# Optimization experiments

Measured on AMD Instinct MI355X. Metric: run time of the kernel, lower is better.

## Reference

```python
import jax, jax.numpy as jnp
import numpy as np

N, E, NNZ = 50000, 10000, 250000   # nodes, hyperedges, incidences
IN_CH, H, D = 128, 64, 6           # in_channels, MLP_hidden, stalk dim
EPS = 1e-5


def setup_inputs() -> dict:
    key = jax.random.key(0)
    ks = jax.random.split(key, 12)
    inp = {}
    inp["x"] = jax.random.normal(ks[0], (N, IN_CH), jnp.float32)
    inp["hyperedge_attr"] = jax.random.normal(ks[1], (E, IN_CH), jnp.float32)  # init_hedge='rand'
    inp["node_idx"] = jax.random.randint(ks[2], (NNZ,), 0, N)
    inp["edge_idx"] = jax.random.randint(ks[3], (NNZ,), 0, E)
    inp["node_types"] = jax.random.randint(ks[4], (N,), 0, 3)
    inp["hyperedge_types"] = jax.random.randint(ks[5], (E,), 0, 6)
    s = 1.0 / np.sqrt(IN_CH)
    inp["W_lin"] = jax.random.uniform(ks[6], (IN_CH, H * D), jnp.float32, -s, s)
    inp["b_lin"] = jnp.zeros((H * D,), jnp.float32)
    inp["ln_g"] = jnp.ones((2 * H,), jnp.float32)
    inp["ln_b"] = jnp.zeros((2 * H,), jnp.float32)
    s2 = 1.0 / np.sqrt(2 * H)
    inp["W_sheaf"] = jax.random.uniform(ks[7], (2 * H, D), jnp.float32, -s2, s2)
    inp["b_sheaf"] = jnp.zeros((D,), jnp.float32)
    s3 = 1.0 / np.sqrt(H)
    inp["W_conv0"] = jax.random.uniform(ks[8], (H, H), jnp.float32, -s3, s3)
    inp["b_conv0"] = jnp.zeros((H,), jnp.float32)
    inp["W_conv1"] = jax.random.uniform(ks[9], (H, H), jnp.float32, -s3, s3)
    inp["b_conv1"] = jnp.zeros((H,), jnp.float32)
    return inp


def _layernorm(x, g, b):
    mu = x.mean(-1, keepdims=True)
    var = ((x - mu) ** 2).mean(-1, keepdims=True)
    return (x - mu) * jax.lax.rsqrt(var + EPS) * g + b


def reference(x, hyperedge_attr, node_idx, edge_idx, node_types, hyperedge_types,
              W_lin, b_lin, ln_g, ln_b, W_sheaf, b_sheaf,
              W_conv0, b_conv0, W_conv1, b_conv1):
    # --- input projection + stalk reshape (self.lin) ---
    xs = (x @ W_lin + b_lin).reshape(N * D, H)              # [N*d, H]
    es = (hyperedge_attr @ W_lin + b_lin).reshape(E * D, H)  # [E*d, H]

    # --- SheafBuilderDiag (local_concat, sigmoid act) ---
    xa = xs.reshape(N, D, H).mean(1)   # [N, H] stalk-averaged node feats
    ea = es.reshape(E, D, H).mean(1)   # [E, H]
    feat = jnp.concatenate([xa[node_idx], ea[edge_idx]], axis=-1)  # [NNZ, 2H]
    alpha = jax.nn.sigmoid(_layernorm(feat, ln_g, ln_b) @ W_sheaf + b_sheaf)  # [NNZ, D]

    dr = jnp.arange(D)
    row_exp = (node_idx[:, None] * D + dr).reshape(-1)  # [NNZ*D] expanded node index
    col_exp = (edge_idx[:, None] * D + dr).reshape(-1)  # [NNZ*D] expanded hyperedge index
    a = alpha.reshape(-1)                               # [NNZ*D]

    # --- degree_norm: D^-1 (nodes) and B^-1 (hyperedges) from incidence counts ---
    ones = jnp.ones_like(a)
    Dn = jax.ops.segment_sum(ones, row_exp, num_segments=N * D)
    Dinv = jnp.where(Dn > 0, 1.0 / Dn, 0.0)
    Bn = jax.ops.segment_sum(ones, col_exp, num_segments=E * D)
    Binv = jnp.where(Bn > 0, 1.0 / Bn, 0.0)

    def conv(xin, W, bias):
        # HyperDiffusionDiagSheafConv: out = xW - D^-1 H^T B^-1 H (xW) + bias
        xl = xin @ W
        m = Binv[:, None] * jax.ops.segment_sum(a[:, None] * xl[row_exp], col_exp, num_segments=E * D)
        agg = Dinv[:, None] * jax.ops.segment_sum(a[:, None] * m[col_exp], row_exp, num_segments=N * D)
        return xl - agg + bias

    h1 = jax.nn.elu(conv(xs, W_conv0, b_conv0))   # dropout inactive (eval)
    h2 = conv(h1, W_conv1, b_conv1)
    return jax.nn.elu(h2.reshape(N, H * D))
```

## Files before the change

### kernel.cpp

```cpp
#include <hip/hip_runtime.h>
#include <hip/hip_bf16.h>

#define N_NODES 50000
#define N_EDGES 10000
#define NNZV    250000
#define IN_CH   128
#define HDIM    64
#define DSTALK  6
#define HD      384
#define NROWS   (N_NODES * DSTALK)
#define EROWS   (N_EDGES * DSTALK)

__global__ __launch_bounds__(256) void k_wefft(
    const float* __restrict__ W_lin, const float* __restrict__ W0,
    float* __restrict__ W0effT) {
  int idx = blockIdx.x * blockDim.x + threadIdx.x;
  if (idx >= IN_CH * HD) return;
  int k = idx / HD, j = idx - k * HD;
  int r = j >> 6, h = j & 63;
  float s = 0.f;
#pragma unroll 8
  for (int m = 0; m < HDIM; m++)
    s += W_lin[k * HD + r * HDIM + m] * W0[m * HDIM + h];
  W0effT[(size_t)j * IN_CH + k] = s;
}

#define WS_BASE (IN_CH * HDIM + HD + HDIM)
#define WS_END  (WS_BASE + 780 + HDIM * HDIM)
__global__ __launch_bounds__(256) void k_wsmall(
    const float* __restrict__ W_lin, const float* __restrict__ b_lin,
    const float* __restrict__ W0, const float* __restrict__ W1,
    const float* __restrict__ g, const float* __restrict__ bln,
    const float* __restrict__ Ws, const float* __restrict__ bs,
    float* __restrict__ Wm, float* __restrict__ cm, float* __restrict__ c0,
    float* __restrict__ gwN, float* __restrict__ gwE,
    float* __restrict__ G, float* __restrict__ K, float* __restrict__ W1T) {
  int idx = blockIdx.x * blockDim.x + threadIdx.x;
  if (idx < IN_CH * HDIM) {
    int k = idx >> 6, h = idx & 63;
    float s = 0.f;
#pragma unroll
    for (int r = 0; r < DSTALK; r++) s += W_lin[k * HD + r * HDIM + h];
    Wm[idx] = s * (1.f / 6.f);
  } else if (idx < IN_CH * HDIM + HD) {
    int j = idx - IN_CH * HDIM;
    int r = j >> 6, h = j & 63;
    float s = 0.f;
#pragma unroll 8
    for (int m = 0; m < HDIM; m++) s += b_lin[r * HDIM + m] * W0[m * HDIM + h];
    c0[j] = s;
  } else if (idx < WS_BASE) {
    int h = idx - IN_CH * HDIM - HD;
    float s = 0.f;
#pragma unroll
    for (int r = 0; r < DSTALK; r++) s += b_lin[r * HDIM + h];
    cm[h] = s * (1.f / 6.f);
  } else if (idx < WS_BASE + 384) {
    int i = idx - WS_BASE;
    int h = i / 6, r = i - h * 6;
    gwN[i] = g[h] * Ws[h * DSTALK + r];
  } else if (idx < WS_BASE + 768) {
    int i = idx - WS_BASE - 384;
    int h = i / 6, r = i - h * 6;
    gwE[i] = g[64 + h] * Ws[(64 + h) * DSTALK + r];
  } else if (idx < WS_BASE + 774) {
    int r = idx - WS_BASE - 768;
    float s = 0.f;
    for (int i = 0; i < 2 * HDIM; i++) s += g[i] * Ws[i * DSTALK + r];
    G[r] = s;
  } else if (idx < WS_BASE + 780) {
    int r = idx - WS_BASE - 774;
    float s = 0.f;
    for (int i = 0; i < 2 * HDIM; i++) s += bln[i] * Ws[i * DSTALK + r];
    K[r] = s + bs[r];
  } else if (idx < WS_END) {
    int i = idx - WS_BASE - 780;
    int c = i >> 6, k = i & 63;
    W1T[c * HDIM + k] = W1[k * HDIM + c];
  }
}

__global__ __launch_bounds__(256) void k_xa_stats(
    const float* __restrict__ x, const float* __restrict__ ea,
    const float* __restrict__ Wm, const float* __restrict__ cm,
    const float* __restrict__ gwN, const float* __restrict__ gwE,
    float* __restrict__ stats) {
  __shared__ float lx[64][IN_CH];
  __shared__ float ox[64][HDIM + 1];
  __shared__ float lgw[2][64 * DSTALK];
  const int row0 = blockIdx.x * 64;
  const int tid = threadIdx.x;
  for (int i = tid; i < 2 * 64 * DSTALK; i += 256) {
    int which = i / 384, k = i - which * 384;
    lgw[which][k] = which ? gwE[k] : gwN[k];
  }
  for (int i = tid; i < 64 * IN_CH; i += 256) {
    int r = i >> 7, k = i & 127;
    int row = row0 + r;
    float v = 0.f;
    if (row < N_NODES) v = x[row * IN_CH + k];
    else if (row < N_NODES + N_EDGES) v = ea[(row - N_NODES) * IN_CH + k];
    lx[r][k] = v;
  }
  __syncthreads();
  const int col = tid & 63, rg = tid >> 6;
  float acc[16];
#pragma unroll
  for (int i = 0; i < 16; i++) acc[i] = 0.f;
  for (int k = 0; k < IN_CH; k++) {
    float w = Wm[k * HDIM + col];
#pragma unroll
    for (int i = 0; i < 16; i++) acc[i] += lx[rg * 16 + i][k] * w;
  }
  const float c = cm[col];
#pragma unroll
  for (int i = 0; i < 16; i++) ox[rg * 16 + i][col] = acc[i] + c;
  __syncthreads();
  for (int t = tid; t < 512; t += 256) {
    int row = t >> 3, st = t & 7;
    int grow = row0 + row;
    if (grow >= N_NODES + N_EDGES) continue;
    const float* __restrict__ gw = (grow >= N_NODES) ? lgw[1] : lgw[0];
    float s = 0.f;
    if (st == 0) {
#pragma unroll 8
      for (int h = 0; h < HDIM; h++) s += ox[row][h];
    } else if (st == 1) {
#pragma unroll 8
      for (int h = 0; h < HDIM; h++) { float v = ox[row][h]; s += v * v; }
    } else {
      int r = st - 2;
#pragma unroll 8
      for (int h = 0; h < HDIM; h++) s += ox[row][h] * gw[h * DSTALK + r];
    }
    stats[(size_t)grow * 8 + st] = s;
  }
}

__global__ __launch_bounds__(256, 2) void k_xl0(
    const float* __restrict__ x, const float* __restrict__ W0effT,
    const float* __restrict__ c0, float* __restrict__ xl0) {
  __shared__ float4 aS[8][129];
  __shared__ float4 bS[8][129];
  const int tid = threadIdx.x;
  const int row0 = blockIdx.x * 128;
  const int col0 = blockIdx.y * 128;
  const int tc = tid & 15, tr = tid >> 4;
  float4 pa[4], pb[4];

#define STAGE_LOAD(kc)                                                        \
  {                                                                           \
    _Pragma("unroll")                                                         \
    for (int i = 0; i < 4; i++) {                                             \
      int fidx = tid + (i << 8);                                              \
      int row = fidx >> 3, kq = fidx & 7;                                     \
      int gk = (kc) * 32 + kq * 4;                                            \
      int grow = row0 + row;                                                  \
      pa[i] = (grow < N_NODES)                                                \
                  ? *(const float4*)(x + (size_t)grow * IN_CH + gk)           \
                  : make_float4(0.f, 0.f, 0.f, 0.f);                          \
      pb[i] = *(const float4*)(W0effT + (size_t)(col0 + row) * IN_CH + gk);   \
    }                                                                         \
  }

  float acc[8][8];
#pragma unroll
  for (int i = 0; i < 8; i++)
#pragma unroll
    for (int j = 0; j < 8; j++) acc[i][j] = 0.f;

  STAGE_LOAD(0);
#pragma unroll 1
  for (int kc = 0; kc < 4; kc++) {
#pragma unroll
    for (int i = 0; i < 4; i++) {
      int fidx = tid + (i << 8);
      int row = fidx >> 3, kq = fidx & 7;
      aS[kq][row] = pa[i];
      bS[kq][row] = pb[i];
    }
    __syncthreads();
    if (kc < 3) STAGE_LOAD(kc + 1);
#pragma unroll 1
    for (int kq = 0; kq < 8; kq++) {
      float4 b[8];
#pragma unroll
      for (int j = 0; j < 8; j++) b[j] = bS[kq][tc + (j << 4)];
#pragma unroll
      for (int i = 0; i < 8; i++) {
        float4 a = aS[kq][tr + (i << 4)];
#pragma unroll
        for (int j = 0; j < 8; j++)
          acc[i][j] += a.x * b[j].x + a.y * b[j].y + a.z * b[j].z + a.w * b[j].w;
      }
    }
    __syncthreads();
  }
#undef STAGE_LOAD

  float cc[8];
#pragma unroll
  for (int j = 0; j < 8; j++) cc[j] = c0[col0 + tc + (j << 4)];
#pragma unroll
  for (int i = 0; i < 8; i++) {
    int row = row0 + tr + (i << 4);
    if (row >= N_NODES) continue;
    float* __restrict__ orow = xl0 + (size_t)row * HD + col0;
#pragma unroll
    for (int j = 0; j < 8; j++) {
      orow[tc + (j << 4)] = acc[i][j] + cc[j];
    }
  }
}

__global__ __launch_bounds__(256) void k_xw(
    const float* __restrict__ xin, const float* __restrict__ W1T,
    float* __restrict__ xl) {
  __shared__ float4 xav[16][65];
  __shared__ float4 wbv[16][65];
  const int tid = threadIdx.x;
  const int row0 = blockIdx.x * 64;
  const int tc = tid & 15, tr = tid >> 4;
#pragma unroll
  for (int i = 0; i < 4; i++) {
    int fidx = tid + i * 256;
    int row = fidx >> 4, kq = fidx & 15;
    int grow = row0 + row;
    float4 v = make_float4(0.f, 0.f, 0.f, 0.f);
    if (grow < NROWS) v = *(const float4*)(xin + (size_t)grow * HDIM + kq * 4);
    xav[kq][row] = v;
    wbv[kq][row] = *(const float4*)(W1T + row * HDIM + kq * 4);
  }
  __syncthreads();
  float acc[4][4] = {{0.f}};
  for (int kq = 0; kq < 16; kq++) {
    float4 xa[4], wb[4];
#pragma unroll
    for (int i = 0; i < 4; i++) xa[i] = xav[kq][tr + (i << 4)];
#pragma unroll
    for (int j = 0; j < 4; j++) wb[j] = wbv[kq][tc + (j << 4)];
#pragma unroll
    for (int i = 0; i < 4; i++)
#pragma unroll
      for (int j = 0; j < 4; j++)
        acc[i][j] += xa[i].x * wb[j].x + xa[i].y * wb[j].y +
                     xa[i].z * wb[j].z + xa[i].w * wb[j].w;
  }
#pragma unroll
  for (int i = 0; i < 4; i++) {
    int row = row0 + tr + (i << 4);
    if (row >= NROWS) continue;
#pragma unroll
    for (int j = 0; j < 4; j++) {
      int col = tc + (j << 4);
      xl[(size_t)row * HDIM + col] = acc[i][j];
    }
  }
}

__global__ __launch_bounds__(256) void k_sheaf2(
    const int* __restrict__ nidx, const int* __restrict__ eidx,
    const float* __restrict__ stats,
    const float* __restrict__ G, const float* __restrict__ K,
    float* __restrict__ alpha) {
  int j = blockIdx.x * blockDim.x + threadIdx.x;
  if (j >= NNZV) return;
  int n = nidx[j], e = eidx[j];
  const float4* __restrict__ sn = (const float4*)(stats + (size_t)n * 8);
  const float4* __restrict__ se = (const float4*)(stats + ((size_t)(N_NODES + e)) * 8);
  float4 a0 = sn[0], a1 = sn[1];
  float4 b0 = se[0], b1 = se[1];
  float mu = (a0.x + b0.x) * (1.f / 128.f);
  float var = (a0.y + b0.y) * (1.f / 128.f) - mu * mu;
  float rs = rsqrtf(var + 1e-5f);
  float p[DSTALK] = {a0.z + b0.z, a0.w + b0.w, a1.x + b1.x,
                     a1.y + b1.y, a1.z + b1.z, a1.w + b1.w};
#pragma unroll
  for (int r = 0; r < DSTALK; r++) {
    float z = rs * (p[r] - mu * G[r]) + K[r];
    alpha[(size_t)j * DSTALK + r] = 1.f / (1.f + expf(-z));
  }
}

__global__ void k_count(const int* __restrict__ nidx, const int* __restrict__ eidx,
                        int* __restrict__ cntN, int* __restrict__ cntE) {
  int j = blockIdx.x * blockDim.x + threadIdx.x;
  if (j < NNZV) {
    atomicAdd(&cntN[nidx[j]], 1);
    atomicAdd(&cntE[eidx[j]], 1);
  }
}

__global__ __launch_bounds__(256) void k_scan_a(
    const int* __restrict__ cnt, int n, int* __restrict__ row,
    int* __restrict__ bsum) {
  const int b = blockIdx.x, t = threadIdx.x;
  const int i0 = b * 512 + 2 * t, i1 = i0 + 1;
  int c0 = (i0 < n) ? cnt[i0] : 0;
  int c1 = (i1 < n) ? cnt[i1] : 0;
  int ts = c0 + c1;
  const int lane = t & 63, wv = t >> 6;
  int s = ts;
#pragma unroll
  for (int o = 1; o < 64; o <<= 1) {
    int v = __shfl_up(s, o);
    if (lane >= o) s += v;
  }
  __shared__ int wsum[4];
  if (lane == 63) wsum[wv] = s;
  __syncthreads();
  int wbase = 0;
#pragma unroll
  for (int wprev = 0; wprev < 3; wprev++)
    if (wprev < wv) wbase += wsum[wprev];
  const int incl = wbase + s;
  const int excl = incl - ts;
  if (i0 < n) row[i0] = excl;
  if (i1 < n) row[i1] = excl + c0;
  if (t == 255) bsum[b] = incl;
}

__global__ __launch_bounds__(128) void k_scan_b(
    const int* __restrict__ bsum, int nb, int* __restrict__ bbase) {
  const int t = threadIdx.x;
  int v = (t < nb) ? bsum[t] : 0;
  const int lane = t & 63, wv = t >> 6;
  int s = v;
#pragma unroll
  for (int o = 1; o < 64; o <<= 1) {
    int u = __shfl_up(s, o);
    if (lane >= o) s += u;
  }
  __shared__ int wsum[2];
  if (lane == 63) wsum[wv] = s;
  __syncthreads();
  const int incl = ((wv == 1) ? wsum[0] : 0) + s;
  if (t < nb) bbase[t] = incl - v;
  if (t == 127) bbase[nb] = incl;
}

__global__ __launch_bounds__(256) void k_scan_c(
    const int* __restrict__ cnt, const int* __restrict__ bbase, int n, int nb,
    int* __restrict__ row, int* __restrict__ fill, float* __restrict__ inv) {
  int i = blockIdx.x * blockDim.x + threadIdx.x;
  if (i < n) {
    int v = row[i] + bbase[i >> 9];
    row[i] = v;
    fill[i] = v;
    int c = cnt[i];
    inv[i] = c > 0 ? 1.f / (float)c : 0.f;
  }
  if (i == 0) row[n] = bbase[nb];
}

__global__ void k_fill(const int* __restrict__ nidx, const int* __restrict__ eidx,
                       int* __restrict__ fillN, int* __restrict__ fillE,
                       int* __restrict__ jlN, int* __restrict__ jlE,
                       int* __restrict__ elN, int* __restrict__ nlE) {
  int j = blockIdx.x * blockDim.x + threadIdx.x;
  if (j < NNZV) {
    int n = nidx[j], e = eidx[j];
    int p = atomicAdd(&fillN[n], 1);
    jlN[p] = j; elN[p] = e;
    int q = atomicAdd(&fillE[e], 1);
    jlE[q] = j; nlE[q] = n;
  }
}

__global__ __launch_bounds__(256) void k_gather_e(
    const int* __restrict__ rowE, const int* __restrict__ jlE,
    const int* __restrict__ nlE, const float* __restrict__ alpha,
    const float* __restrict__ xl, const float* __restrict__ Binv,
    float* __restrict__ msum) {
  int e = (blockIdx.x * blockDim.x + threadIdx.x) >> 6;
  int lane = threadIdx.x & 63;
  if (e >= N_EDGES) return;
  float acc[DSTALK];
#pragma unroll
  for (int r = 0; r < DSTALK; r++) acc[r] = 0.f;
  const int lo = rowE[e], hi = rowE[e + 1];
  for (int p = lo; p < hi; p++) {
    const int j = jlE[p];
    const int n = nlE[p];
    const float* __restrict__ xr = xl + (size_t)n * HD + lane;
    const float* __restrict__ ar = alpha + (size_t)j * DSTALK;
#pragma unroll
    for (int r = 0; r < DSTALK; r++) acc[r] += ar[r] * xr[r * HDIM];
  }
  const float bv = Binv[e];
  float* __restrict__ mr = msum + (size_t)e * HD + lane;
#pragma unroll
  for (int r = 0; r < DSTALK; r++) mr[r * HDIM] = acc[r] * bv;
}

__global__ __launch_bounds__(256) void k_gather_n(
    const int* __restrict__ rowN, const int* __restrict__ jlN,
    const int* __restrict__ elN, const float* __restrict__ alpha,
    const float* __restrict__ msum, const float* __restrict__ Dinv,
    const float* __restrict__ xl, const float* __restrict__ bias,
    float* __restrict__ outp) {
  int n = (blockIdx.x * blockDim.x + threadIdx.x) >> 6;
  int lane = threadIdx.x & 63;
  if (n >= N_NODES) return;
  float acc[DSTALK];
#pragma unroll
  for (int r = 0; r < DSTALK; r++) acc[r] = 0.f;
  const int lo = rowN[n], hi = rowN[n + 1];
  for (int p = lo; p < hi; p++) {
    const int j = jlN[p];
    const int e = elN[p];
    const float* __restrict__ mr = msum + (size_t)e * HD + lane;
    const float* __restrict__ ar = alpha + (size_t)j * DSTALK;
#pragma unroll
    for (int r = 0; r < DSTALK; r++) acc[r] += ar[r] * mr[r * HDIM];
  }
  const float dv = Dinv[n];
  const float bb = bias[lane];
  const float* __restrict__ xr = xl + (size_t)n * HD + lane;
  float* __restrict__ orow = outp + (size_t)n * HD + lane;
#pragma unroll
  for (int r = 0; r < DSTALK; r++) {
    float v = xr[r * HDIM] + bb - dv * acc[r];
    orow[r * HDIM] = v > 0.f ? v : expm1f(v);
  }
}

extern "C" void kernel_launch(void* const* d_in, const int* in_sizes, int n_in,
                              void* d_out, int out_size, void* d_ws, size_t ws_size,
                              hipStream_t stream) {
  const float* x    = (const float*)d_in[0];
  const float* hea  = (const float*)d_in[1];
  const int*  nidx  = (const int*)d_in[2];
  const int*  eidx  = (const int*)d_in[3];
  const float* W_lin = (const float*)d_in[6];
  const float* b_lin = (const float*)d_in[7];
  const float* ln_g  = (const float*)d_in[8];
  const float* ln_b  = (const float*)d_in[9];
  const float* W_sh  = (const float*)d_in[10];
  const float* b_sh  = (const float*)d_in[11];
  const float* W_c0  = (const float*)d_in[12];
  const float* b_c0  = (const float*)d_in[13];
  const float* W_c1  = (const float*)d_in[14];
  const float* b_c1  = (const float*)d_in[15];
  float* out = (float*)d_out;

  char* ws = (char*)d_ws;
  size_t off = 0;
  auto alloc = [&](size_t bytes) {
    size_t o = off;
    off = (off + bytes + 255) & ~(size_t)255;
    return o;
  };
  size_t o_xl0   = alloc((size_t)NROWS * HDIM * 4);
  size_t o_msum  = alloc((size_t)EROWS * HDIM * 4);
  size_t o_alpha = alloc((size_t)NNZV * DSTALK * 4);
  size_t o_stats = alloc((size_t)(N_NODES + N_EDGES) * 8 * 4);
  size_t o_jlN   = alloc((size_t)NNZV * 4);
  size_t o_jlE   = alloc((size_t)NNZV * 4);
  size_t o_elN   = alloc((size_t)NNZV * 4);
  size_t o_nlE   = alloc((size_t)NNZV * 4);
  size_t o_cntN  = alloc((size_t)N_NODES * 4);
  size_t o_cntE  = alloc((size_t)N_EDGES * 4);
  size_t o_rowN  = alloc((size_t)(N_NODES + 1) * 4);
  size_t o_rowE  = alloc((size_t)(N_EDGES + 1) * 4);
  size_t o_filN  = alloc((size_t)N_NODES * 4);
  size_t o_filE  = alloc((size_t)N_EDGES * 4);
  size_t o_Dinv  = alloc((size_t)N_NODES * 4);
  size_t o_Binv  = alloc((size_t)N_EDGES * 4);
  size_t o_bsN   = alloc((size_t)256 * 4);
  size_t o_bbN   = alloc((size_t)256 * 4);
  size_t o_bsE   = alloc((size_t)256 * 4);
  size_t o_bbE   = alloc((size_t)256 * 4);
  size_t o_WeffT = alloc((size_t)IN_CH * HD * 4);
  size_t o_Wm    = alloc((size_t)IN_CH * HDIM * 4);
  size_t o_cm    = alloc((size_t)HDIM * 4);
  size_t o_c0    = alloc((size_t)HD * 4);
  size_t o_gwN   = alloc((size_t)64 * DSTALK * 4);
  size_t o_gwE   = alloc((size_t)64 * DSTALK * 4);
  size_t o_G     = alloc((size_t)DSTALK * 4);
  size_t o_K     = alloc((size_t)DSTALK * 4);
  size_t o_W1T   = alloc((size_t)HDIM * HDIM * 4);

  float* xl0    = (float*)(ws + o_xl0);
  float* msum   = (float*)(ws + o_msum);
  float* alpha  = (float*)(ws + o_alpha);
  float* stats  = (float*)(ws + o_stats);
  int*   jlN    = (int*)(ws + o_jlN);
  int*   jlE    = (int*)(ws + o_jlE);
  int*   elN    = (int*)(ws + o_elN);
  int*   nlE    = (int*)(ws + o_nlE);
  int*   cntN   = (int*)(ws + o_cntN);
  int*   cntE   = (int*)(ws + o_cntE);
  int*   rowN   = (int*)(ws + o_rowN);
  int*   rowE   = (int*)(ws + o_rowE);
  int*   filN   = (int*)(ws + o_filN);
  int*   filE   = (int*)(ws + o_filE);
  float* Dinv   = (float*)(ws + o_Dinv);
  float* Binv   = (float*)(ws + o_Binv);
  int*   bsN    = (int*)(ws + o_bsN);
  int*   bbN    = (int*)(ws + o_bbN);
  int*   bsE    = (int*)(ws + o_bsE);
  int*   bbE    = (int*)(ws + o_bbE);
  float* W0effT = (float*)(ws + o_WeffT);
  float* Wm     = (float*)(ws + o_Wm);
  float* cm     = (float*)(ws + o_cm);
  float* c0     = (float*)(ws + o_c0);
  float* gwN    = (float*)(ws + o_gwN);
  float* gwE    = (float*)(ws + o_gwE);
  float* G      = (float*)(ws + o_G);
  float* K      = (float*)(ws + o_K);
  float* W1T    = (float*)(ws + o_W1T);

  const int NB_N = (N_NODES + 511) / 512;
  const int NB_E = (N_EDGES + 511) / 512;

  k_wefft<<<(IN_CH * HD + 255) / 256, 256, 0, stream>>>(W_lin, W_c0, W0effT);
  k_wsmall<<<(WS_END + 255) / 256, 256, 0, stream>>>(
      W_lin, b_lin, W_c0, W_c1, ln_g, ln_b, W_sh, b_sh,
      Wm, cm, c0, gwN, gwE, G, K, W1T);

  hipMemsetAsync(ws + o_cntN, 0, (size_t)N_NODES * 4, stream);
  hipMemsetAsync(ws + o_cntE, 0, (size_t)N_EDGES * 4, stream);
  k_count<<<(NNZV + 255) / 256, 256, 0, stream>>>(nidx, eidx, cntN, cntE);
  k_scan_a<<<NB_N, 256, 0, stream>>>(cntN, N_NODES, rowN, bsN);
  k_scan_a<<<NB_E, 256, 0, stream>>>(cntE, N_EDGES, rowE, bsE);
  k_scan_b<<<1, 128, 0, stream>>>(bsN, NB_N, bbN);
  k_scan_b<<<1, 128, 0, stream>>>(bsE, NB_E, bbE);
  k_scan_c<<<(N_NODES + 255) / 256, 256, 0, stream>>>(cntN, bbN, N_NODES, NB_N,
                                                      rowN, filN, Dinv);
  k_scan_c<<<(N_EDGES + 255) / 256, 256, 0, stream>>>(cntE, bbE, N_EDGES, NB_E,
                                                      rowE, filE, Binv);
  k_fill<<<(NNZV + 255) / 256, 256, 0, stream>>>(nidx, eidx, filN, filE,
                                                 jlN, jlE, elN, nlE);

  k_xa_stats<<<(N_NODES + N_EDGES + 63) / 64, 256, 0, stream>>>(
      x, hea, Wm, cm, gwN, gwE, stats);

  k_sheaf2<<<(NNZV + 255) / 256, 256, 0, stream>>>(nidx, eidx, stats, G, K, alpha);

  {
    dim3 g((N_NODES + 127) / 128, HD / 128);
    k_xl0<<<g, 256, 0, stream>>>(x, W0effT, c0, xl0);
  }
  k_gather_e<<<(N_EDGES + 3) / 4, 256, 0, stream>>>(rowE, jlE, nlE, alpha, xl0, Binv, msum);
  k_gather_n<<<(N_NODES + 3) / 4, 256, 0, stream>>>(rowN, jlN, elN, alpha, msum, Dinv,
                                                    xl0, b_c0, xl0);

  k_xw<<<(NROWS + 63) / 64, 256, 0, stream>>>(xl0, W1T, xl0);
  k_gather_e<<<(N_EDGES + 3) / 4, 256, 0, stream>>>(rowE, jlE, nlE, alpha, xl0, Binv, msum);
  k_gather_n<<<(N_NODES + 3) / 4, 256, 0, stream>>>(rowN, jlN, elN, alpha, msum, Dinv,
                                                    xl0, b_c1, out);

  (void)in_sizes; (void)n_in; (void)out_size; (void)ws_size;
}
```

Baseline: 693.0 us.

## Shrink xl0 GEMM row tile to 64 and drop register prefetch staging

The node-projection GEMM now uses 64-row tiles instead of 128, so each thread holds a 4x8 accumulator. It also drops the register double-buffered prefetch in favour of loading each k-chunk straight into shared memory, and removes the launch-bounds occupancy hint. Fewer registers and twice as many blocks should raise occupancy and spread the work across more CUs. The cost is less reuse of each B tile and no overlap of global loads with compute inside a block.

After: 670.1 us. 1.03x faster.

```diff
diff --git a/kernel.cpp b/kernel.cpp
--- a/kernel.cpp
+++ b/kernel.cpp
@@ -137,72 +137,61 @@
   }
 }
 
-__global__ __launch_bounds__(256, 2) void k_xl0(
+__global__ __launch_bounds__(256) void k_xl0(
     const float* __restrict__ x, const float* __restrict__ W0effT,
     const float* __restrict__ c0, float* __restrict__ xl0) {
-  __shared__ float4 aS[8][129];
+  __shared__ float4 aS[8][65];
   __shared__ float4 bS[8][129];
   const int tid = threadIdx.x;
-  const int row0 = blockIdx.x * 128;
+  const int row0 = blockIdx.x * 64;
   const int col0 = blockIdx.y * 128;
   const int tc = tid & 15, tr = tid >> 4;
-  float4 pa[4], pb[4];
-
-#define STAGE_LOAD(kc)                                                        \
-  {                                                                           \
-    _Pragma("unroll")                                                         \
-    for (int i = 0; i < 4; i++) {                                             \
-      int fidx = tid + (i << 8);                                              \
-      int row = fidx >> 3, kq = fidx & 7;                                     \
-      int gk = (kc) * 32 + kq * 4;                                            \
-      int grow = row0 + row;                                                  \
-      pa[i] = (grow < N_NODES)                                                \
-                  ? *(const float4*)(x + (size_t)grow * IN_CH + gk)           \
-                  : make_float4(0.f, 0.f, 0.f, 0.f);                          \
-      pb[i] = *(const float4*)(W0effT + (size_t)(col0 + row) * IN_CH + gk);   \
-    }                                                                         \
-  }
-
-  float acc[8][8];
-#pragma unroll
-  for (int i = 0; i < 8; i++)
+  float acc[4][8];
+#pragma unroll
+  for (int i = 0; i < 4; i++)
 #pragma unroll
     for (int j = 0; j < 8; j++) acc[i][j] = 0.f;
 
-  STAGE_LOAD(0);
 #pragma unroll 1
   for (int kc = 0; kc < 4; kc++) {
-#pragma unroll
-    for (int i = 0; i < 4; i++) {
+    if (kc) __syncthreads();
+#pragma unroll
+    for (int i = 0; i < 6; i++) {
       int fidx = tid + (i << 8);
-      int row = fidx >> 3, kq = fidx & 7;
-      aS[kq][row] = pa[i];
-      bS[kq][row] = pb[i];
+      int kq = fidx & 7, rc = fidx >> 3;
+      int gk = kc * 32 + kq * 4;
+      if (rc < 64) {
+        int grow = row0 + rc;
+        float4 v = (grow < N_NODES)
+                       ? *(const float4*)(x + (size_t)grow * IN_CH + gk)
+                       : make_float4(0.f, 0.f, 0.f, 0.f);
+        aS[kq][rc] = v;
+      } else {
+        bS[kq][rc - 64] =
+            *(const float4*)(W0effT + (size_t)(col0 + rc - 64) * IN_CH + gk);
+      }
     }
     __syncthreads();
-    if (kc < 3) STAGE_LOAD(kc + 1);
 #pragma unroll 1
     for (int kq = 0; kq < 8; kq++) {
       float4 b[8];
 #pragma unroll
       for (int j = 0; j < 8; j++) b[j] = bS[kq][tc + (j << 4)];
 #pragma unroll
-      for (int i = 0; i < 8; i++) {
+      for (int i = 0; i < 4; i++) {
         float4 a = aS[kq][tr + (i << 4)];
 #pragma unroll
         for (int j = 0; j < 8; j++)
           acc[i][j] += a.x * b[j].x + a.y * b[j].y + a.z * b[j].z + a.w * b[j].w;
       }
     }
-    __syncthreads();
-  }
-#undef STAGE_LOAD
+  }
 
   float cc[8];
 #pragma unroll
   for (int j = 0; j < 8; j++) cc[j] = c0[col0 + tc + (j << 4)];
 #pragma unroll
-  for (int i = 0; i < 8; i++) {
+  for (int i = 0; i < 4; i++) {
     int row = row0 + tr + (i << 4);
     if (row >= N_NODES) continue;
     float* __restrict__ orow = xl0 + (size_t)row * HD + col0;
@@ -539,7 +528,7 @@
   k_sheaf2<<<(NNZV + 255) / 256, 256, 0, stream>>>(nidx, eidx, stats, G, K, alpha);
 
   {
-    dim3 g((N_NODES + 127) / 128, HD / 128);
+    dim3 g((N_NODES + 63) / 64, HD / 128);
     k_xl0<<<g, 256, 0, stream>>>(x, W0effT, c0, xl0);
   }
   k_gather_e<<<(N_EDGES + 3) / 4, 256, 0, stream>>>(rowE, jlE, nlE, alpha, xl0, Binv, msum);
```
